# Performance work log

Measured on AMD Instinct MI355X. Metric: run time of the kernel, lower is better.

Reference implementation:

```python
import jax, jax.numpy as jnp
import numpy as np

N = 50000
E = 800000
IN_CH = 256
HID = 32
HEADS = 4
OUT_CH = 40
NEG_SLOPE = 0.2
BN_EPS = 1e-5


def _gat_conv(x, W, att_src, att_dst, bias, src, dst, num_nodes, concat):
    # x: [N, F_in]; W: [F_in, H*C]; att_src/att_dst: [H, C]
    H, C = att_src.shape
    h = (x @ W).reshape(num_nodes, H, C)            # [N, H, C]
    a_src = (h * att_src[None]).sum(-1)             # [N, H]
    a_dst = (h * att_dst[None]).sum(-1)             # [N, H]
    e = jax.nn.leaky_relu(a_src[src] + a_dst[dst], NEG_SLOPE)  # [Etot, H]
    # segment softmax over incoming edges of each destination node
    m = jax.ops.segment_max(e, dst, num_segments=num_nodes)    # [N, H]
    ex = jnp.exp(e - m[dst])
    s = jax.ops.segment_sum(ex, dst, num_segments=num_nodes)   # [N, H]
    alpha = ex / (s[dst] + 1e-16)                   # [Etot, H]
    out = jax.ops.segment_sum(h[src] * alpha[:, :, None], dst,
                              num_segments=num_nodes)          # [N, H, C]
    out = out.reshape(num_nodes, H * C) if concat else out.mean(axis=1)
    return out + bias


def setup_inputs() -> dict:
    key = jax.random.key(0)
    ks = jax.random.split(key, 12)
    x = jax.random.normal(ks[0], (N, IN_CH), dtype=jnp.float32)
    edge_index = jax.random.randint(ks[1], (2, E), 0, N, dtype=jnp.int64)
    # layer 1: in -> heads*hid, concat
    W1 = jax.random.normal(ks[2], (IN_CH, HEADS * HID), dtype=jnp.float32) * (1.0 / np.sqrt(IN_CH))
    att_src1 = jax.random.normal(ks[3], (HEADS, HID), dtype=jnp.float32) * 0.1
    att_dst1 = jax.random.normal(ks[4], (HEADS, HID), dtype=jnp.float32) * 0.1
    b1 = jnp.zeros((HEADS * HID,), dtype=jnp.float32)
    # batch norm over hidden*heads features
    gamma = jnp.ones((HEADS * HID,), dtype=jnp.float32)
    beta = jnp.zeros((HEADS * HID,), dtype=jnp.float32)
    # layer 2: heads*hid -> out, heads=1, mean (concat=False)
    W2 = jax.random.normal(ks[5], (HEADS * HID, OUT_CH), dtype=jnp.float32) * (1.0 / np.sqrt(HEADS * HID))
    att_src2 = jax.random.normal(ks[6], (1, OUT_CH), dtype=jnp.float32) * 0.1
    att_dst2 = jax.random.normal(ks[7], (1, OUT_CH), dtype=jnp.float32) * 0.1
    b2 = jnp.zeros((OUT_CH,), dtype=jnp.float32)
    return {"x": x, "edge_index": edge_index, "W1": W1, "att_src1": att_src1,
            "att_dst1": att_dst1, "b1": b1, "gamma": gamma, "beta": beta,
            "W2": W2, "att_src2": att_src2, "att_dst2": att_dst2, "b2": b2}


def reference(x, edge_index, W1, att_src1, att_dst1, b1, gamma, beta,
              W2, att_src2, att_dst2, b2):
    num_nodes = x.shape[0]
    loops = jnp.arange(num_nodes, dtype=edge_index.dtype)
    src = jnp.concatenate([edge_index[0], loops])   # add self-loops (PyG default)
    dst = jnp.concatenate([edge_index[1], loops])
    h = _gat_conv(x, W1, att_src1, att_dst1, b1, src, dst, num_nodes, concat=True)
    # BatchNorm over nodes (training-mode batch statistics)
    mu = h.mean(axis=0)
    var = h.var(axis=0)
    h = (h - mu) * jax.lax.rsqrt(var + BN_EPS) * gamma + beta
    h = jax.nn.elu(h)
    out = _gat_conv(h, W2, att_src2, att_dst2, b2, src, dst, num_nodes, concat=False)
    return out
```

## Files before the change

### kernel.cpp

```cpp
#include <hip/hip_runtime.h>

#define NN 50000
#define EE 800000
#define FIN 256
#define F1 128
#define F2 40
#define CAP 48
#define G1B ((NN + 127) / 128)
#define FILLB ((EE + 255) / 256)
#define G1PB 3126
#define G2B ((NN + 15) / 16)

typedef unsigned int u32;
typedef unsigned short u16;

static __device__ __forceinline__ u32 f2bf(float f) {
  u32 u = __float_as_uint(f);
  return (u + 0x7FFFu + ((u >> 16) & 1u)) >> 16;
}
#define BF_LO(u) __uint_as_float((u) << 16)
#define BF_HI(u) __uint_as_float((u) & 0xFFFF0000u)

__global__ __launch_bounds__(256) void g1f_kernel(const float* __restrict__ x,
                                                  const float* __restrict__ W1,
                                                  const float* __restrict__ att_src,
                                                  const float* __restrict__ att_dst,
                                                  u32* __restrict__ h1bf,
                                                  float* __restrict__ a_src,
                                                  float* __restrict__ a_dst,
                                                  const int* __restrict__ ei,
                                                  int* __restrict__ cnt,
                                                  int* __restrict__ csr) {
  __shared__ float Alds[16 * 132];
  __shared__ float Blds[16 * 128];
  __shared__ float att_s[128], att_d[128];
  const int t = threadIdx.x;

  if (blockIdx.x >= G1B) {
    int e = (blockIdx.x - G1B) * 256 + t;
    if (e < EE) {
      int src = ei[e];
      int dst = ei[EE + e];
      int p = atomicAdd(cnt + dst, 1);
      if (p < CAP) csr[dst * CAP + p] = src;
    }
    return;
  }

  if (t < 128) { att_s[t] = att_src[t]; att_d[t] = att_dst[t]; }
  const int m0 = blockIdx.x * 128;
  const int arow = t >> 1;
  const int akk = (t & 1) * 8;
  const int brow = t >> 4;
  const int bc = (t & 15) * 8;
  const int ty = t >> 4;
  const int tx = t & 15;

  float acc[8][8];
#pragma unroll
  for (int i = 0; i < 8; ++i)
#pragma unroll
    for (int j = 0; j < 8; ++j) acc[i][j] = 0.f;

  for (int k0 = 0; k0 < FIN; k0 += 16) {
    float4 a0 = {0.f, 0.f, 0.f, 0.f}, a1 = {0.f, 0.f, 0.f, 0.f};
    int gr = m0 + arow;
    if (gr < NN) {
      a0 = *(const float4*)(x + (size_t)gr * FIN + k0 + akk);
      a1 = *(const float4*)(x + (size_t)gr * FIN + k0 + akk + 4);
    }
    float4 b0 = *(const float4*)(W1 + (size_t)(k0 + brow) * F1 + bc);
    float4 b1 = *(const float4*)(W1 + (size_t)(k0 + brow) * F1 + bc + 4);
    __syncthreads();
    Alds[(akk + 0) * 132 + arow] = a0.x;
    Alds[(akk + 1) * 132 + arow] = a0.y;
    Alds[(akk + 2) * 132 + arow] = a0.z;
    Alds[(akk + 3) * 132 + arow] = a0.w;
    Alds[(akk + 4) * 132 + arow] = a1.x;
    Alds[(akk + 5) * 132 + arow] = a1.y;
    Alds[(akk + 6) * 132 + arow] = a1.z;
    Alds[(akk + 7) * 132 + arow] = a1.w;
    *(float4*)(Blds + brow * 128 + bc) = b0;
    *(float4*)(Blds + brow * 128 + bc + 4) = b1;
    __syncthreads();
#pragma unroll
    for (int k = 0; k < 16; ++k) {
      float4 av0 = *(const float4*)(Alds + k * 132 + ty * 8);
      float4 av1 = *(const float4*)(Alds + k * 132 + ty * 8 + 4);
      float4 bv0 = *(const float4*)(Blds + k * 128 + tx * 8);
      float4 bv1 = *(const float4*)(Blds + k * 128 + tx * 8 + 4);
      float aa[8] = {av0.x, av0.y, av0.z, av0.w, av1.x, av1.y, av1.z, av1.w};
      float bb[8] = {bv0.x, bv0.y, bv0.z, bv0.w, bv1.x, bv1.y, bv1.z, bv1.w};
#pragma unroll
      for (int i = 0; i < 8; ++i)
#pragma unroll
        for (int j = 0; j < 8; ++j) acc[i][j] = fmaf(aa[i], bb[j], acc[i][j]);
    }
  }
#pragma unroll
  for (int i = 0; i < 8; ++i) {
    int gr = m0 + ty * 8 + i;
    if (gr < NN) {
      uint4 w;
      w.x = f2bf(acc[i][0]) | (f2bf(acc[i][1]) << 16);
      w.y = f2bf(acc[i][2]) | (f2bf(acc[i][3]) << 16);
      w.z = f2bf(acc[i][4]) | (f2bf(acc[i][5]) << 16);
      w.w = f2bf(acc[i][6]) | (f2bf(acc[i][7]) << 16);
      *(uint4*)(h1bf + ((size_t)(tx >> 2) * NN + gr) * 16 + (tx & 3) * 4) = w;
    }
  }
#pragma unroll
  for (int i = 0; i < 8; ++i) {
    float ps = 0.f, pd = 0.f;
#pragma unroll
    for (int j = 0; j < 8; ++j) {
      int c = tx * 8 + j;
      ps += acc[i][j] * att_s[c];
      pd += acc[i][j] * att_d[c];
    }
    ps += __shfl_xor(ps, 1); pd += __shfl_xor(pd, 1);
    ps += __shfl_xor(ps, 2); pd += __shfl_xor(pd, 2);
    if ((tx & 3) == 0) {
      int gr = m0 + ty * 8 + i;
      if (gr < NN) {
        int head = tx >> 2;
        a_src[gr * 4 + head] = ps;
        a_dst[gr * 4 + head] = pd;
      }
    }
  }
}

__global__ __launch_bounds__(256) void gather1_kernel(const int* __restrict__ cnt,
                                                      const int* __restrict__ csr,
                                                      const float* __restrict__ a_src,
                                                      const float* __restrict__ a_dst,
                                                      const u32* __restrict__ h1bf,
                                                      const float* __restrict__ b1,
                                                      float* __restrict__ h1b,
                                                      float* __restrict__ bnsum,
                                                      float* __restrict__ bnsq) {
  __shared__ float bns[32], bnq[32];
  int t = threadIdx.x;
  if (t < 32) { bns[t] = 0.f; bnq[t] = 0.f; }
  __syncthreads();
  int d = blockIdx.x;
  int xcd = d & 7;
  int p = xcd >> 1;
  int nb = ((d >> 3) << 1) + (xcd & 1);
  int n = nb * 16 + (t >> 4);
  int sub = t & 15;
  int g = sub >> 2;
  int l = sub & 3;
  int f0 = p * 32 + l * 8;
  float acc[8] = {0.f, 0.f, 0.f, 0.f, 0.f, 0.f, 0.f, 0.f};
  float ssum = 0.f;
  if (n < NN) {
    float adst = a_dst[n * 4 + p];
    const u32* hb = h1bf + (size_t)p * NN * 16 + l * 4;
    if (g == 0) {
      float e0 = a_src[n * 4 + p] + adst;
      e0 = e0 > 0.f ? e0 : 0.2f * e0;
      float x0 = __expf(e0);
      uint4 q = *(const uint4*)(hb + (size_t)n * 16);
      acc[0] = fmaf(x0, BF_LO(q.x), acc[0]); acc[1] = fmaf(x0, BF_HI(q.x), acc[1]);
      acc[2] = fmaf(x0, BF_LO(q.y), acc[2]); acc[3] = fmaf(x0, BF_HI(q.y), acc[3]);
      acc[4] = fmaf(x0, BF_LO(q.z), acc[4]); acc[5] = fmaf(x0, BF_HI(q.z), acc[5]);
      acc[6] = fmaf(x0, BF_LO(q.w), acc[6]); acc[7] = fmaf(x0, BF_HI(q.w), acc[7]);
      ssum += x0;
    }
    const int* row = csr + n * CAP;
    int m = cnt[n]; if (m > CAP) m = CAP;
    int i = g;
    for (; i + 4 < m; i += 8) {
      int s0 = row[i];
      int s1 = row[i + 4];
      float e0 = a_src[s0 * 4 + p] + adst;
      float e1 = a_src[s1 * 4 + p] + adst;
      uint4 q0 = *(const uint4*)(hb + (size_t)s0 * 16);
      uint4 q1 = *(const uint4*)(hb + (size_t)s1 * 16);
      e0 = e0 > 0.f ? e0 : 0.2f * e0;  float x0 = __expf(e0);
      e1 = e1 > 0.f ? e1 : 0.2f * e1;  float x1 = __expf(e1);
      acc[0] = fmaf(x0, BF_LO(q0.x), acc[0]); acc[1] = fmaf(x0, BF_HI(q0.x), acc[1]);
      acc[2] = fmaf(x0, BF_LO(q0.y), acc[2]); acc[3] = fmaf(x0, BF_HI(q0.y), acc[3]);
      acc[4] = fmaf(x0, BF_LO(q0.z), acc[4]); acc[5] = fmaf(x0, BF_HI(q0.z), acc[5]);
      acc[6] = fmaf(x0, BF_LO(q0.w), acc[6]); acc[7] = fmaf(x0, BF_HI(q0.w), acc[7]);
      acc[0] = fmaf(x1, BF_LO(q1.x), acc[0]); acc[1] = fmaf(x1, BF_HI(q1.x), acc[1]);
      acc[2] = fmaf(x1, BF_LO(q1.y), acc[2]); acc[3] = fmaf(x1, BF_HI(q1.y), acc[3]);
      acc[4] = fmaf(x1, BF_LO(q1.z), acc[4]); acc[5] = fmaf(x1, BF_HI(q1.z), acc[5]);
      acc[6] = fmaf(x1, BF_LO(q1.w), acc[6]); acc[7] = fmaf(x1, BF_HI(q1.w), acc[7]);
      ssum += x0 + x1;
    }
    for (; i < m; i += 4) {
      int s0 = row[i];
      float e0 = a_src[s0 * 4 + p] + adst;
      e0 = e0 > 0.f ? e0 : 0.2f * e0;
      float x0 = __expf(e0);
      uint4 q = *(const uint4*)(hb + (size_t)s0 * 16);
      acc[0] = fmaf(x0, BF_LO(q.x), acc[0]); acc[1] = fmaf(x0, BF_HI(q.x), acc[1]);
      acc[2] = fmaf(x0, BF_LO(q.y), acc[2]); acc[3] = fmaf(x0, BF_HI(q.y), acc[3]);
      acc[4] = fmaf(x0, BF_LO(q.z), acc[4]); acc[5] = fmaf(x0, BF_HI(q.z), acc[5]);
      acc[6] = fmaf(x0, BF_LO(q.w), acc[6]); acc[7] = fmaf(x0, BF_HI(q.w), acc[7]);
      ssum += x0;
    }
  }
#pragma unroll
  for (int j = 0; j < 8; ++j) {
    acc[j] += __shfl_xor(acc[j], 4);
    acc[j] += __shfl_xor(acc[j], 8);
  }
  ssum += __shfl_xor(ssum, 4);
  ssum += __shfl_xor(ssum, 8);
  if (n < NN && g == 0) {
    float inv = 1.f / (ssum + 1e-16f);
    float4 b0 = *(const float4*)(b1 + f0);
    float4 b4 = *(const float4*)(b1 + f0 + 4);
    float o[8];
    o[0] = acc[0] * inv + b0.x; o[1] = acc[1] * inv + b0.y;
    o[2] = acc[2] * inv + b0.z; o[3] = acc[3] * inv + b0.w;
    o[4] = acc[4] * inv + b4.x; o[5] = acc[5] * inv + b4.y;
    o[6] = acc[6] * inv + b4.z; o[7] = acc[7] * inv + b4.w;
    float4 w0 = {o[0], o[1], o[2], o[3]};
    float4 w1 = {o[4], o[5], o[6], o[7]};
    *(float4*)(h1b + (size_t)n * F1 + f0) = w0;
    *(float4*)(h1b + (size_t)n * F1 + f0 + 4) = w1;
    int lb = l * 8;
#pragma unroll
    for (int j = 0; j < 8; ++j) {
      atomicAdd(&bns[lb + j], o[j]);
      atomicAdd(&bnq[lb + j], o[j] * o[j]);
    }
  }
  __syncthreads();
  if (t < 32) {
    atomicAdd(bnsum + p * 32 + t, bns[t]);
    atomicAdd(bnsq + p * 32 + t, bnq[t]);
  }
}

__global__ __launch_bounds__(256) void gemm2_kernel(const float* __restrict__ hpre,
                                                    const float* __restrict__ W2,
                                                    const float* __restrict__ bnsum,
                                                    const float* __restrict__ bnsq,
                                                    const float* __restrict__ gamma,
                                                    const float* __restrict__ beta,
                                                    u16* __restrict__ h2a,
                                                    u16* __restrict__ h2b,
                                                    const float* __restrict__ att_src2,
                                                    const float* __restrict__ att_dst2,
                                                    float* __restrict__ a_src2,
                                                    float* __restrict__ a_dst2) {
  __shared__ float Wlds[128 * 40];
  __shared__ float Alds[16 * 128];
  __shared__ float sc[128], sh[128];
  int t = threadIdx.x;
  for (int i = t; i < 128 * 40; i += 256) Wlds[i] = W2[i];
  if (t < 128) {
    const float invN = 1.f / (float)NN;
    float mu = bnsum[t] * invN;
    float var = bnsq[t] * invN - mu * mu;
    float s = gamma[t] * rsqrtf(var + 1e-5f);
    sc[t] = s;
    sh[t] = beta[t] - mu * s;
  }
  int tr = t >> 3;
  int tc = t & 7;
  float as5[5], ad5[5];
#pragma unroll
  for (int j = 0; j < 5; ++j) { as5[j] = att_src2[tc * 5 + j]; ad5[j] = att_dst2[tc * 5 + j]; }
  int n0 = blockIdx.x * 128;
  int lrow = t >> 1;
  int lkk = (t & 1) * 8;
  float acc[4][5];
#pragma unroll
  for (int i = 0; i < 4; ++i)
#pragma unroll
    for (int j = 0; j < 5; ++j) acc[i][j] = 0.f;

  for (int k0 = 0; k0 < F1; k0 += 16) {
    float av[8];
    int gn = n0 + lrow;
    if (gn < NN) {
      float4 v0 = *(const float4*)(hpre + (size_t)gn * F1 + k0 + lkk);
      float4 v1 = *(const float4*)(hpre + (size_t)gn * F1 + k0 + lkk + 4);
      av[0] = v0.x; av[1] = v0.y; av[2] = v0.z; av[3] = v0.w;
      av[4] = v1.x; av[5] = v1.y; av[6] = v1.z; av[7] = v1.w;
    } else {
#pragma unroll
      for (int j = 0; j < 8; ++j) av[j] = 0.f;
    }
    __syncthreads();
#pragma unroll
    for (int j = 0; j < 8; ++j) {
      int kg = k0 + lkk + j;
      float a = av[j] * sc[kg] + sh[kg];
      a = a > 0.f ? a : (__expf(a) - 1.f);
      Alds[(lkk + j) * 128 + lrow] = a;
    }
    __syncthreads();
#pragma unroll
    for (int k = 0; k < 16; ++k) {
      float4 a4 = *(const float4*)(Alds + k * 128 + tr * 4);
      float aa[4] = {a4.x, a4.y, a4.z, a4.w};
      float w[5];
#pragma unroll
      for (int j = 0; j < 5; ++j) w[j] = Wlds[(k0 + k) * 40 + tc * 5 + j];
#pragma unroll
      for (int i = 0; i < 4; ++i)
#pragma unroll
        for (int j = 0; j < 5; ++j) acc[i][j] = fmaf(aa[i], w[j], acc[i][j]);
    }
  }
#pragma unroll
  for (int i = 0; i < 4; ++i) {
    int gn = n0 + tr * 4 + i;
    if (gn < NN) {
#pragma unroll
      for (int j = 0; j < 5; ++j) {
        int f = tc * 5 + j;
        u16 v = (u16)f2bf(acc[i][j]);
        if (f < 32) h2a[(size_t)gn * 32 + f] = v;
        else        h2b[(size_t)gn * 8 + (f - 32)] = v;
      }
    }
  }
#pragma unroll
  for (int i = 0; i < 4; ++i) {
    float ps = 0.f, pd = 0.f;
#pragma unroll
    for (int j = 0; j < 5; ++j) { ps += acc[i][j] * as5[j]; pd += acc[i][j] * ad5[j]; }
#pragma unroll
    for (int off = 1; off < 8; off <<= 1) {
      ps += __shfl_xor(ps, off);
      pd += __shfl_xor(pd, off);
    }
    if (tc == 0) {
      int gn = n0 + tr * 4 + i;
      if (gn < NN) { a_src2[gn] = ps; a_dst2[gn] = pd; }
    }
  }
}

__global__ __launch_bounds__(256) void gather2_kernel(const int* __restrict__ cnt,
                                                      const int* __restrict__ csr,
                                                      const float* __restrict__ a_src,
                                                      const float* __restrict__ a_dst,
                                                      const u32* __restrict__ h2a,
                                                      const u32* __restrict__ h2b,
                                                      const float* __restrict__ b2,
                                                      float* __restrict__ out) {
  int t = threadIdx.x;
  int n = blockIdx.x * 16 + (t >> 4);
  if (n >= NN) return;
  int l = t & 7;
  int g = (t >> 3) & 1;
  bool act = (l < 5);
  bool isA = (l < 4);
  float adst = a_dst[n];
  float acc[8] = {0.f, 0.f, 0.f, 0.f, 0.f, 0.f, 0.f, 0.f};
  float ssum = 0.f;
  const uint4 zz = {0u, 0u, 0u, 0u};
  if (g == 0) {
    float e0 = a_src[n] + adst;
    e0 = e0 > 0.f ? e0 : 0.2f * e0;
    float x0 = __expf(e0);
    uint4 q = act ? (isA ? *(const uint4*)(h2a + (size_t)n * 16 + l * 4)
                         : *(const uint4*)(h2b + (size_t)n * 4)) : zz;
    acc[0] = fmaf(x0, BF_LO(q.x), acc[0]); acc[1] = fmaf(x0, BF_HI(q.x), acc[1]);
    acc[2] = fmaf(x0, BF_LO(q.y), acc[2]); acc[3] = fmaf(x0, BF_HI(q.y), acc[3]);
    acc[4] = fmaf(x0, BF_LO(q.z), acc[4]); acc[5] = fmaf(x0, BF_HI(q.z), acc[5]);
    acc[6] = fmaf(x0, BF_LO(q.w), acc[6]); acc[7] = fmaf(x0, BF_HI(q.w), acc[7]);
    ssum += x0;
  }
  const int* row = csr + n * CAP;
  int m = cnt[n]; if (m > CAP) m = CAP;
  for (int c = 4 * g; c < m; c += 8) {
    if (c + 4 <= m) {
      int4 s4 = *(const int4*)(row + c);
      float e0 = a_src[s4.x] + adst;
      float e1 = a_src[s4.y] + adst;
      float e2 = a_src[s4.z] + adst;
      float e3 = a_src[s4.w] + adst;
      uint4 q0 = act ? (isA ? *(const uint4*)(h2a + (size_t)s4.x * 16 + l * 4)
                            : *(const uint4*)(h2b + (size_t)s4.x * 4)) : zz;
      uint4 q1 = act ? (isA ? *(const uint4*)(h2a + (size_t)s4.y * 16 + l * 4)
                            : *(const uint4*)(h2b + (size_t)s4.y * 4)) : zz;
      uint4 q2 = act ? (isA ? *(const uint4*)(h2a + (size_t)s4.z * 16 + l * 4)
                            : *(const uint4*)(h2b + (size_t)s4.z * 4)) : zz;
      uint4 q3 = act ? (isA ? *(const uint4*)(h2a + (size_t)s4.w * 16 + l * 4)
                            : *(const uint4*)(h2b + (size_t)s4.w * 4)) : zz;
      e0 = e0 > 0.f ? e0 : 0.2f * e0;  float x0 = __expf(e0);
      e1 = e1 > 0.f ? e1 : 0.2f * e1;  float x1 = __expf(e1);
      e2 = e2 > 0.f ? e2 : 0.2f * e2;  float x2 = __expf(e2);
      e3 = e3 > 0.f ? e3 : 0.2f * e3;  float x3 = __expf(e3);
      acc[0] = fmaf(x0, BF_LO(q0.x), acc[0]); acc[1] = fmaf(x0, BF_HI(q0.x), acc[1]);
      acc[2] = fmaf(x0, BF_LO(q0.y), acc[2]); acc[3] = fmaf(x0, BF_HI(q0.y), acc[3]);
      acc[4] = fmaf(x0, BF_LO(q0.z), acc[4]); acc[5] = fmaf(x0, BF_HI(q0.z), acc[5]);
      acc[6] = fmaf(x0, BF_LO(q0.w), acc[6]); acc[7] = fmaf(x0, BF_HI(q0.w), acc[7]);
      acc[0] = fmaf(x1, BF_LO(q1.x), acc[0]); acc[1] = fmaf(x1, BF_HI(q1.x), acc[1]);
      acc[2] = fmaf(x1, BF_LO(q1.y), acc[2]); acc[3] = fmaf(x1, BF_HI(q1.y), acc[3]);
      acc[4] = fmaf(x1, BF_LO(q1.z), acc[4]); acc[5] = fmaf(x1, BF_HI(q1.z), acc[5]);
      acc[6] = fmaf(x1, BF_LO(q1.w), acc[6]); acc[7] = fmaf(x1, BF_HI(q1.w), acc[7]);
      acc[0] = fmaf(x2, BF_LO(q2.x), acc[0]); acc[1] = fmaf(x2, BF_HI(q2.x), acc[1]);
      acc[2] = fmaf(x2, BF_LO(q2.y), acc[2]); acc[3] = fmaf(x2, BF_HI(q2.y), acc[3]);
      acc[4] = fmaf(x2, BF_LO(q2.z), acc[4]); acc[5] = fmaf(x2, BF_HI(q2.z), acc[5]);
      acc[6] = fmaf(x2, BF_LO(q2.w), acc[6]); acc[7] = fmaf(x2, BF_HI(q2.w), acc[7]);
      acc[0] = fmaf(x3, BF_LO(q3.x), acc[0]); acc[1] = fmaf(x3, BF_HI(q3.x), acc[1]);
      acc[2] = fmaf(x3, BF_LO(q3.y), acc[2]); acc[3] = fmaf(x3, BF_HI(q3.y), acc[3]);
      acc[4] = fmaf(x3, BF_LO(q3.z), acc[4]); acc[5] = fmaf(x3, BF_HI(q3.z), acc[5]);
      acc[6] = fmaf(x3, BF_LO(q3.w), acc[6]); acc[7] = fmaf(x3, BF_HI(q3.w), acc[7]);
      ssum += x0 + x1 + x2 + x3;
    } else {
      for (int i = c; i < m; ++i) {
        int s0 = row[i];
        float e0 = a_src[s0] + adst;
        e0 = e0 > 0.f ? e0 : 0.2f * e0;
        float x0 = __expf(e0);
        uint4 q = act ? (isA ? *(const uint4*)(h2a + (size_t)s0 * 16 + l * 4)
                             : *(const uint4*)(h2b + (size_t)s0 * 4)) : zz;
        acc[0] = fmaf(x0, BF_LO(q.x), acc[0]); acc[1] = fmaf(x0, BF_HI(q.x), acc[1]);
        acc[2] = fmaf(x0, BF_LO(q.y), acc[2]); acc[3] = fmaf(x0, BF_HI(q.y), acc[3]);
        acc[4] = fmaf(x0, BF_LO(q.z), acc[4]); acc[5] = fmaf(x0, BF_HI(q.z), acc[5]);
        acc[6] = fmaf(x0, BF_LO(q.w), acc[6]); acc[7] = fmaf(x0, BF_HI(q.w), acc[7]);
        ssum += x0;
      }
    }
  }
#pragma unroll
  for (int j = 0; j < 8; ++j) acc[j] += __shfl_xor(acc[j], 8);
  ssum += __shfl_xor(ssum, 8);
  float inv = 1.f / (ssum + 1e-16f);
  if (g == 0 && act) {
    float* op = out + (size_t)n * F2 + l * 8;
#pragma unroll
    for (int j = 0; j < 8; ++j) op[j] = acc[j] * inv + b2[l * 8 + j];
  }
}

extern "C" void kernel_launch(void* const* d_in, const int* in_sizes, int n_in,
                              void* d_out, int out_size, void* d_ws, size_t ws_size,
                              hipStream_t stream) {
  const float* x        = (const float*)d_in[0];
  const int*   ei       = (const int*)d_in[1];
  const float* W1       = (const float*)d_in[2];
  const float* att_src1 = (const float*)d_in[3];
  const float* att_dst1 = (const float*)d_in[4];
  const float* b1       = (const float*)d_in[5];
  const float* gamma    = (const float*)d_in[6];
  const float* beta     = (const float*)d_in[7];
  const float* W2       = (const float*)d_in[8];
  const float* att_src2 = (const float*)d_in[9];
  const float* att_dst2 = (const float*)d_in[10];
  const float* b2       = (const float*)d_in[11];
  float* out = (float*)d_out;

  int* cnt      = (int*)d_ws;
  float* bnsum  = (float*)(cnt + 50048);
  float* bnsq   = bnsum + 128;
  int* csr      = (int*)(bnsq + 128);
  u32* h1bf     = (u32*)(csr + NN * CAP);
  float* h1b    = (float*)(h1bf + 3200000);
  u32* h2a      = (u32*)(h1b + 6400000);
  u32* h2b      = h2a + 800000;
  float* a_src1 = (float*)(h2b + 200000);
  float* a_dst1 = a_src1 + 200000;
  float* a_src2 = a_dst1 + 200000;
  float* a_dst2 = a_src2 + 50000;

  hipMemsetAsync(cnt, 0, (50048 + 256) * sizeof(int), stream);

  g1f_kernel<<<G1B + FILLB, 256, 0, stream>>>(x, W1, att_src1, att_dst1,
                                              h1bf, a_src1, a_dst1,
                                              ei, cnt, csr);
  gather1_kernel<<<(G1PB / 2) * 8, 256, 0, stream>>>(cnt, csr, a_src1, a_dst1,
                                                     h1bf, b1, h1b, bnsum, bnsq);
  gemm2_kernel<<<(NN + 127) / 128, 256, 0, stream>>>(h1b, W2, bnsum, bnsq,
                                                     gamma, beta,
                                                     (u16*)h2a, (u16*)h2b,
                                                     att_src2, att_dst2,
                                                     a_src2, a_dst2);
  gather2_kernel<<<G2B, 256, 0, stream>>>(cnt, csr, a_src2, a_dst2,
                                          h2a, h2b, b2, out);
}
```

Before: 313.1 us.

## Compute layer-1 projection with fp16 MFMA and register-prefetched tiles

Replaces the fp32 FMA register-tiled GEMM for x@W1 with fp16 MFMA 16x16x32 instructions on 64-row tiles. The next K-slice of x and W1 is prefetched into registers while the current one is computed. The attention logits are then reduced across lanes with shuffles, and h1 is stored element-wise as bf16. This aims to cut the FP32 ALU cost of the GEMM, at the price of fp16 input rounding and more grid blocks.

```diff
diff --git a/kernel.cpp b/kernel.cpp
--- a/kernel.cpp
+++ b/kernel.cpp
@@ -6,13 +6,16 @@
 #define F1 128
 #define F2 40
 #define CAP 48
-#define G1B ((NN + 127) / 128)
+#define G1B ((NN + 63) / 64)
 #define FILLB ((EE + 255) / 256)
 #define G1PB 3126
 #define G2B ((NN + 15) / 16)
+#define LSTR 56
 
 typedef unsigned int u32;
 typedef unsigned short u16;
+typedef _Float16 h8 __attribute__((ext_vector_type(8)));
+typedef float f4 __attribute__((ext_vector_type(4)));
 
 static __device__ __forceinline__ u32 f2bf(float f) {
   u32 u = __float_as_uint(f);
@@ -31,9 +34,8 @@
                                                   const int* __restrict__ ei,
                                                   int* __restrict__ cnt,
                                                   int* __restrict__ csr) {
-  __shared__ float Alds[16 * 132];
-  __shared__ float Blds[16 * 128];
-  __shared__ float att_s[128], att_d[128];
+  __shared__ __align__(16) _Float16 Alds[64 * LSTR];
+  __shared__ __align__(16) _Float16 Blds[128 * LSTR];
   const int t = threadIdx.x;
 
   if (blockIdx.x >= G1B) {
@@ -47,86 +49,113 @@
     return;
   }
 
-  if (t < 128) { att_s[t] = att_src[t]; att_d[t] = att_dst[t]; }
-  const int m0 = blockIdx.x * 128;
-  const int arow = t >> 1;
-  const int akk = (t & 1) * 8;
-  const int brow = t >> 4;
-  const int bc = (t & 15) * 8;
-  const int ty = t >> 4;
-  const int tx = t & 15;
-
-  float acc[8][8];
-#pragma unroll
-  for (int i = 0; i < 8; ++i)
-#pragma unroll
-    for (int j = 0; j < 8; ++j) acc[i][j] = 0.f;
-
-  for (int k0 = 0; k0 < FIN; k0 += 16) {
-    float4 a0 = {0.f, 0.f, 0.f, 0.f}, a1 = {0.f, 0.f, 0.f, 0.f};
+  const int m0 = blockIdx.x * 64;
+  const int l  = t & 63;
+  const int w  = t >> 6;
+  const int q  = l & 15;
+  const int hq = l >> 4;
+
+  const int arow  = t >> 2;
+  const int akoff = (t & 3) * 8;
+  const int bn    = t & 127;
+  const int bkh   = (t >> 7) * 16;
+
+  f4 acc[8] = {};
+
+  float ax[8];
+  float bx[16];
+  {
     int gr = m0 + arow;
     if (gr < NN) {
-      a0 = *(const float4*)(x + (size_t)gr * FIN + k0 + akk);
-      a1 = *(const float4*)(x + (size_t)gr * FIN + k0 + akk + 4);
-    }
-    float4 b0 = *(const float4*)(W1 + (size_t)(k0 + brow) * F1 + bc);
-    float4 b1 = *(const float4*)(W1 + (size_t)(k0 + brow) * F1 + bc + 4);
+      float4 u0 = *(const float4*)(x + (size_t)gr * FIN + akoff);
+      float4 u1 = *(const float4*)(x + (size_t)gr * FIN + akoff + 4);
+      ax[0] = u0.x; ax[1] = u0.y; ax[2] = u0.z; ax[3] = u0.w;
+      ax[4] = u1.x; ax[5] = u1.y; ax[6] = u1.z; ax[7] = u1.w;
+    } else {
+#pragma unroll
+      for (int i = 0; i < 8; ++i) ax[i] = 0.f;
+    }
+#pragma unroll
+    for (int i = 0; i < 16; ++i) bx[i] = W1[(size_t)(bkh + i) * F1 + bn];
+  }
+
+  for (int s = 0; s < 8; ++s) {
     __syncthreads();
-    Alds[(akk + 0) * 132 + arow] = a0.x;
-    Alds[(akk + 1) * 132 + arow] = a0.y;
-    Alds[(akk + 2) * 132 + arow] = a0.z;
-    Alds[(akk + 3) * 132 + arow] = a0.w;
-    Alds[(akk + 4) * 132 + arow] = a1.x;
-    Alds[(akk + 5) * 132 + arow] = a1.y;
-    Alds[(akk + 6) * 132 + arow] = a1.z;
-    Alds[(akk + 7) * 132 + arow] = a1.w;
-    *(float4*)(Blds + brow * 128 + bc) = b0;
-    *(float4*)(Blds + brow * 128 + bc + 4) = b1;
+    {
+      h8 av;
+#pragma unroll
+      for (int i = 0; i < 8; ++i) av[i] = (_Float16)ax[i];
+      *(h8*)(Alds + arow * LSTR + akoff) = av;
+      h8 bv0, bv1;
+#pragma unroll
+      for (int i = 0; i < 8; ++i) { bv0[i] = (_Float16)bx[i]; bv1[i] = (_Float16)bx[8 + i]; }
+      *(h8*)(Blds + bn * LSTR + bkh) = bv0;
+      *(h8*)(Blds + bn * LSTR + bkh + 8) = bv1;
+    }
     __syncthreads();
-#pragma unroll
-    for (int k = 0; k < 16; ++k) {
-      float4 av0 = *(const float4*)(Alds + k * 132 + ty * 8);
-      float4 av1 = *(const float4*)(Alds + k * 132 + ty * 8 + 4);
-      float4 bv0 = *(const float4*)(Blds + k * 128 + tx * 8);
-      float4 bv1 = *(const float4*)(Blds + k * 128 + tx * 8 + 4);
-      float aa[8] = {av0.x, av0.y, av0.z, av0.w, av1.x, av1.y, av1.z, av1.w};
-      float bb[8] = {bv0.x, bv0.y, bv0.z, bv0.w, bv1.x, bv1.y, bv1.z, bv1.w};
-#pragma unroll
-      for (int i = 0; i < 8; ++i)
-#pragma unroll
-        for (int j = 0; j < 8; ++j) acc[i][j] = fmaf(aa[i], bb[j], acc[i][j]);
-    }
-  }
-#pragma unroll
-  for (int i = 0; i < 8; ++i) {
-    int gr = m0 + ty * 8 + i;
-    if (gr < NN) {
-      uint4 w;
-      w.x = f2bf(acc[i][0]) | (f2bf(acc[i][1]) << 16);
-      w.y = f2bf(acc[i][2]) | (f2bf(acc[i][3]) << 16);
-      w.z = f2bf(acc[i][4]) | (f2bf(acc[i][5]) << 16);
-      w.w = f2bf(acc[i][6]) | (f2bf(acc[i][7]) << 16);
-      *(uint4*)(h1bf + ((size_t)(tx >> 2) * NN + gr) * 16 + (tx & 3) * 4) = w;
-    }
-  }
-#pragma unroll
-  for (int i = 0; i < 8; ++i) {
-    float ps = 0.f, pd = 0.f;
-#pragma unroll
-    for (int j = 0; j < 8; ++j) {
-      int c = tx * 8 + j;
-      ps += acc[i][j] * att_s[c];
-      pd += acc[i][j] * att_d[c];
-    }
-    ps += __shfl_xor(ps, 1); pd += __shfl_xor(pd, 1);
-    ps += __shfl_xor(ps, 2); pd += __shfl_xor(pd, 2);
-    if ((tx & 3) == 0) {
-      int gr = m0 + ty * 8 + i;
+    if (s < 7) {
+      int k0 = (s + 1) * 32;
+      int gr = m0 + arow;
       if (gr < NN) {
-        int head = tx >> 2;
-        a_src[gr * 4 + head] = ps;
-        a_dst[gr * 4 + head] = pd;
+        float4 u0 = *(const float4*)(x + (size_t)gr * FIN + k0 + akoff);
+        float4 u1 = *(const float4*)(x + (size_t)gr * FIN + k0 + akoff + 4);
+        ax[0] = u0.x; ax[1] = u0.y; ax[2] = u0.z; ax[3] = u0.w;
+        ax[4] = u1.x; ax[5] = u1.y; ax[6] = u1.z; ax[7] = u1.w;
+      } else {
+#pragma unroll
+        for (int i = 0; i < 8; ++i) ax[i] = 0.f;
       }
+#pragma unroll
+      for (int i = 0; i < 16; ++i) bx[i] = W1[(size_t)(k0 + bkh + i) * F1 + bn];
+    }
+    h8 af = *(const h8*)(Alds + (w * 16 + q) * LSTR + hq * 8);
+#pragma unroll
+    for (int nf = 0; nf < 8; ++nf) {
+      h8 bf = *(const h8*)(Blds + (nf * 16 + q) * LSTR + hq * 8);
+      acc[nf] = __builtin_amdgcn_mfma_f32_16x16x32_f16(af, bf, acc[nf], 0, 0, 0);
+    }
+  }
+
+  u16* h1u = (u16*)h1bf;
+#pragma unroll
+  for (int nf = 0; nf < 8; ++nf) {
+    int ph = nf >> 1;
+#pragma unroll
+    for (int r = 0; r < 4; ++r) {
+      int grow = m0 + w * 16 + hq * 4 + r;
+      if (grow < NN)
+        h1u[((size_t)ph * NN + grow) * 32 + (nf & 1) * 16 + q] = (u16)f2bf(acc[nf][r]);
+    }
+  }
+  float as8[8], ad8[8];
+#pragma unroll
+  for (int nf = 0; nf < 8; ++nf) {
+    as8[nf] = att_src[nf * 16 + q];
+    ad8[nf] = att_dst[nf * 16 + q];
+  }
+#pragma unroll
+  for (int r = 0; r < 4; ++r) {
+    float p0 = acc[0][r] * as8[0] + acc[1][r] * as8[1];
+    float p1 = acc[2][r] * as8[2] + acc[3][r] * as8[3];
+    float p2 = acc[4][r] * as8[4] + acc[5][r] * as8[5];
+    float p3 = acc[6][r] * as8[6] + acc[7][r] * as8[7];
+    float d0 = acc[0][r] * ad8[0] + acc[1][r] * ad8[1];
+    float d1 = acc[2][r] * ad8[2] + acc[3][r] * ad8[3];
+    float d2 = acc[4][r] * ad8[4] + acc[5][r] * ad8[5];
+    float d3 = acc[6][r] * ad8[6] + acc[7][r] * ad8[7];
+#pragma unroll
+    for (int off = 1; off < 16; off <<= 1) {
+      p0 += __shfl_xor(p0, off); p1 += __shfl_xor(p1, off);
+      p2 += __shfl_xor(p2, off); p3 += __shfl_xor(p3, off);
+      d0 += __shfl_xor(d0, off); d1 += __shfl_xor(d1, off);
+      d2 += __shfl_xor(d2, off); d3 += __shfl_xor(d3, off);
+    }
+    int grow = m0 + w * 16 + hq * 4 + r;
+    if (grow < NN && q < 8) {
+      float vs = (q & 2) ? ((q & 1) ? p3 : p2) : ((q & 1) ? p1 : p0);
+      float vd = (q & 2) ? ((q & 1) ? d3 : d2) : ((q & 1) ? d1 : d0);
+      if (q < 4) a_src[grow * 4 + q] = vs;
+      else       a_dst[grow * 4 + (q - 4)] = vd;
     }
   }
 }
@@ -162,11 +191,11 @@
       float e0 = a_src[n * 4 + p] + adst;
       e0 = e0 > 0.f ? e0 : 0.2f * e0;
       float x0 = __expf(e0);
-      uint4 q = *(const uint4*)(hb + (size_t)n * 16);
-      acc[0] = fmaf(x0, BF_LO(q.x), acc[0]); acc[1] = fmaf(x0, BF_HI(q.x), acc[1]);
-      acc[2] = fmaf(x0, BF_LO(q.y), acc[2]); acc[3] = fmaf(x0, BF_HI(q.y), acc[3]);
-      acc[4] = fmaf(x0, BF_LO(q.z), acc[4]); acc[5] = fmaf(x0, BF_HI(q.z), acc[5]);
-      acc[6] = fmaf(x0, BF_LO(q.w), acc[6]); acc[7] = fmaf(x0, BF_HI(q.w), acc[7]);
+      uint4 qv = *(const uint4*)(hb + (size_t)n * 16);
+      acc[0] = fmaf(x0, BF_LO(qv.x), acc[0]); acc[1] = fmaf(x0, BF_HI(qv.x), acc[1]);
+      acc[2] = fmaf(x0, BF_LO(qv.y), acc[2]); acc[3] = fmaf(x0, BF_HI(qv.y), acc[3]);
+      acc[4] = fmaf(x0, BF_LO(qv.z), acc[4]); acc[5] = fmaf(x0, BF_HI(qv.z), acc[5]);
+      acc[6] = fmaf(x0, BF_LO(qv.w), acc[6]); acc[7] = fmaf(x0, BF_HI(qv.w), acc[7]);
       ssum += x0;
     }
     const int* row = csr + n * CAP;
@@ -196,11 +225,11 @@
       float e0 = a_src[s0 * 4 + p] + adst;
       e0 = e0 > 0.f ? e0 : 0.2f * e0;
       float x0 = __expf(e0);
-      uint4 q = *(const uint4*)(hb + (size_t)s0 * 16);
-      acc[0] = fmaf(x0, BF_LO(q.x), acc[0]); acc[1] = fmaf(x0, BF_HI(q.x), acc[1]);
-      acc[2] = fmaf(x0, BF_LO(q.y), acc[2]); acc[3] = fmaf(x0, BF_HI(q.y), acc[3]);
-      acc[4] = fmaf(x0, BF_LO(q.z), acc[4]); acc[5] = fmaf(x0, BF_HI(q.z), acc[5]);
-      acc[6] = fmaf(x0, BF_LO(q.w), acc[6]); acc[7] = fmaf(x0, BF_HI(q.w), acc[7]);
+      uint4 qv = *(const uint4*)(hb + (size_t)s0 * 16);
+      acc[0] = fmaf(x0, BF_LO(qv.x), acc[0]); acc[1] = fmaf(x0, BF_HI(qv.x), acc[1]);
+      acc[2] = fmaf(x0, BF_LO(qv.y), acc[2]); acc[3] = fmaf(x0, BF_HI(qv.y), acc[3]);
+      acc[4] = fmaf(x0, BF_LO(qv.z), acc[4]); acc[5] = fmaf(x0, BF_HI(qv.z), acc[5]);
+      acc[6] = fmaf(x0, BF_LO(qv.w), acc[6]); acc[7] = fmaf(x0, BF_HI(qv.w), acc[7]);
       ssum += x0;
     }
   }
```

Result: no change. 313.1 us (+0.0%).
